# Kernel tuning notes

Measured on AMD Instinct MI355X. Metric: run time of the kernel, lower is better.

## Reference

```python
import jax, jax.numpy as jnp
import numpy as np

B, T, C = 2, 2048, 1024
H, HD = 16, 64
M = 256  # per memory bank
K_CANON = 4


def setup_inputs() -> dict:
    key = jax.random.key(0)
    ks = jax.random.split(key, 10)
    s = 0.02
    return {
        "x": jax.random.normal(ks[0], (B, T, C), jnp.float32),
        "fwd_mem": jax.random.normal(ks[1], (B, M, C), jnp.float32),
        "rev_mem": jax.random.normal(ks[2], (B, M, C), jnp.float32),
        "Wq": jax.random.normal(ks[3], (C, C), jnp.float32) * s,
        "Wk": jax.random.normal(ks[4], (C, C), jnp.float32) * s,
        "Wv": jax.random.normal(ks[5], (C, C), jnp.float32) * s,
        "Wo": jax.random.normal(ks[6], (C, C), jnp.float32) * s,
        "gate_w": jax.random.normal(ks[7], (H, C), jnp.float32) * s,
        "gate_b": jnp.zeros((H,), jnp.float32),
        "canon_w": jax.random.normal(ks[8], (C, 1, K_CANON), jnp.float32) * s,
        "canon_bias": jax.random.normal(ks[9], (C,), jnp.float32) * s,
    }


def _canon_conv(y, canon_w, canon_bias):
    # causal depthwise conv1d with residual; torch weight [C,1,K] -> WIO kernel [K,1,C]
    kern = jnp.transpose(canon_w, (2, 1, 0))
    y_pad = jnp.pad(y, ((0, 0), (K_CANON - 1, 0), (0, 0)))
    conv = jax.lax.conv_general_dilated(
        y_pad, kern, window_strides=(1,), padding='VALID',
        dimension_numbers=('NWC', 'WIO', 'NWC'), feature_group_count=C)
    return y + conv + canon_bias


def reference(x, fwd_mem, rev_mem, Wq, Wk, Wv, Wo, gate_w, gate_b, canon_w, canon_bias):
    Bn, Tn, Cn = x.shape
    scale = 1.0 / np.sqrt(HD)

    q = x @ Wq.T  # [B,T,C]
    k = x @ Wk.T
    v = x @ Wv.T
    # memory integration: project memories with same k/v proj, concat on seq dim
    k = jnp.concatenate([k, fwd_mem @ Wk.T, rev_mem @ Wk.T], axis=1)  # [B,S,C]
    v = jnp.concatenate([v, fwd_mem @ Wv.T, rev_mem @ Wv.T], axis=1)
    S = k.shape[1]
    mem_len = S - Tn

    def heads(t):
        return t.reshape(Bn, -1, H, HD).transpose(0, 2, 1, 3)  # [B,h,S,hd]

    qh, kh, vh = heads(q), heads(k), heads(v)
    scores = jnp.einsum('bhtd,bhsd->bhts', qh, kh) * scale  # [B,h,T,S]
    # causal mask over the first T key columns; memory columns fully visible
    causal = jnp.triu(jnp.ones((Tn, Tn), bool), k=1)
    full_mask = jnp.pad(causal, ((0, 0), (0, mem_len)))  # [T,S]
    scores = jnp.where(full_mask[None, None], -jnp.inf, scores)
    w = jax.nn.softmax(scores, axis=-1)

    # split chunk vs memory, gate memory contribution per head
    w_chunk, w_mem = w[..., :Tn], w[..., Tn:]
    v_chunk, v_mem = vh[:, :, :Tn], vh[:, :, Tn:]
    Y_chunk = jnp.einsum('bhts,bhsd->bhtd', w_chunk, v_chunk)
    Y_mem = jnp.einsum('bhtm,bhmd->bhtd', w_mem, v_mem)
    g = jax.nn.sigmoid(q @ gate_w.T + gate_b)  # [B,T,h]
    g = g.transpose(0, 2, 1)[..., None]  # [B,h,T,1]
    Y = Y_chunk + g * Y_mem

    attn_out = Y.transpose(0, 2, 1, 3).reshape(Bn, Tn, Cn)
    attn_out = _canon_conv(attn_out, canon_w, canon_bias)
    return attn_out @ Wo.T
```

## Files before the change

### kernel.cpp

```cpp
#include <hip/hip_runtime.h>
#include <hip/hip_bf16.h>
#include <cstdint>


typedef __bf16 bf16x8_t __attribute__((ext_vector_type(8)));
typedef __bf16 bf16x4_t __attribute__((ext_vector_type(4)));
typedef float f32x4_t __attribute__((ext_vector_type(4)));

__device__ __forceinline__ f32x4_t mfma16(bf16x8_t a, bf16x8_t b, f32x4_t c) {
    return __builtin_amdgcn_mfma_f32_16x16x32_bf16(a, b, c, 0, 0, 0);
}

__device__ __forceinline__ void gl2lds16(const void* g, void* l) {
    __builtin_amdgcn_global_load_lds(
        (__attribute__((address_space(1))) uint32_t*)(uintptr_t)g,
        (__attribute__((address_space(3))) uint32_t*)l, 16, 0, 0);
}

#define OFF_X   0
#define OFF_FWD 4194304
#define OFF_REV 4718592
#define OFF_WQ  5242880
#define OFF_WK  6291456
#define OFF_WV  7340032
#define OFF_WO  8388608
#define OFF_GW  9437184
#define OFF_GB  9453568
#define OFF_CW  9453584
#define OFF_CB  9457680
#define N_TOT   9458704

__global__ __launch_bounds__(256) void conv_all_kernel(
    const void* p0, const void* p1, const void* p2, const void* p3,
    const void* p4, const void* p5, const void* p6, const void* p7,
    const void* p8, const void* p9, const void* p10,
    __hip_bfloat16* __restrict__ arena)
{
    const int i = (blockIdx.x * 256 + threadIdx.x) * 4;
    if (i >= N_TOT) return;
    const void* src; int off;
    if      (i < OFF_FWD) { src = p0;  off = OFF_X;   }
    else if (i < OFF_REV) { src = p1;  off = OFF_FWD; }
    else if (i < OFF_WQ)  { src = p2;  off = OFF_REV; }
    else if (i < OFF_WK)  { src = p3;  off = OFF_WQ;  }
    else if (i < OFF_WV)  { src = p4;  off = OFF_WK;  }
    else if (i < OFF_WO)  { src = p5;  off = OFF_WV;  }
    else if (i < OFF_GW)  { src = p6;  off = OFF_WO;  }
    else if (i < OFF_GB)  { src = p7;  off = OFF_GW;  }
    else if (i < OFF_CW)  { src = p8;  off = OFF_GB;  }
    else if (i < OFF_CB)  { src = p9;  off = OFF_CW;  }
    else                  { src = p10; off = OFF_CB;  }
    const int j = i - off;
    const float4 f = *(const float4*)((const float*)src + j);
    arena[i + 0] = __float2bfloat16(f.x);
    arena[i + 1] = __float2bfloat16(f.y);
    arena[i + 2] = __float2bfloat16(f.z);
    arena[i + 3] = __float2bfloat16(f.w);
}

__device__ __forceinline__ void gemm_core(
    const __hip_bfloat16* __restrict__ A, const __hip_bfloat16* __restrict__ B,
    void* __restrict__ C, int ldc, int f32o, int arow0, int brow0,
    __hip_bfloat16* As, __hip_bfloat16* Bs)
{
    const int tid  = threadIdx.x;
    const int lane = tid & 63;
    const int wid  = tid >> 6;
    const int q4   = lane >> 4;
    const int c16  = lane & 15;
    const int wm   = (wid >> 1) * 64;
    const int wn   = (wid & 1) * 64;
    const int c0 = tid;
    const int c1 = tid + 256;
    const __hip_bfloat16* gA0 = A + (size_t)(arow0 + (c0 >> 2)) * 1024 + ((c0 & 3) << 3);
    const __hip_bfloat16* gA1 = A + (size_t)(arow0 + (c1 >> 2)) * 1024 + ((c1 & 3) << 3);
    const __hip_bfloat16* gB0 = B + (size_t)(brow0 + (c0 >> 2)) * 1024 + ((c0 & 3) << 3);
    const __hip_bfloat16* gB1 = B + (size_t)(brow0 + (c1 >> 2)) * 1024 + ((c1 & 3) << 3);

    f32x4_t acc[4][4];
#pragma unroll
    for (int i = 0; i < 4; ++i)
#pragma unroll
        for (int j = 0; j < 4; ++j)
#pragma unroll
            for (int r = 0; r < 4; ++r) acc[i][j][r] = 0.0f;

    gl2lds16(gA0, As + c0 * 8);
    gl2lds16(gA1, As + c1 * 8);
    gl2lds16(gB0, Bs + c0 * 8);
    gl2lds16(gB1, Bs + c1 * 8);

    for (int it = 0; it < 32; ++it) {
        __hip_bfloat16* curA = As + (it & 1) * 4096;
        __hip_bfloat16* curB = Bs + (it & 1) * 4096;
        __syncthreads();
        if (it < 31) {
            const int nk = (it + 1) * 32;
            __hip_bfloat16* nA = As + ((it + 1) & 1) * 4096;
            __hip_bfloat16* nB = Bs + ((it + 1) & 1) * 4096;
            gl2lds16(gA0 + nk, nA + c0 * 8);
            gl2lds16(gA1 + nk, nA + c1 * 8);
            gl2lds16(gB0 + nk, nB + c0 * 8);
            gl2lds16(gB1 + nk, nB + c1 * 8);
        }
        bf16x8_t af[4], bfr[4];
#pragma unroll
        for (int i = 0; i < 4; ++i)
            af[i] = *(const bf16x8_t*)&curA[(wm + i * 16 + c16) * 32 + q4 * 8];
#pragma unroll
        for (int j = 0; j < 4; ++j)
            bfr[j] = *(const bf16x8_t*)&curB[(wn + j * 16 + c16) * 32 + q4 * 8];
#pragma unroll
        for (int i = 0; i < 4; ++i)
#pragma unroll
            for (int j = 0; j < 4; ++j)
                acc[i][j] = mfma16(af[i], bfr[j], acc[i][j]);
    }
#pragma unroll
    for (int i = 0; i < 4; ++i) {
        const int mg = arow0 + wm + i * 16 + q4 * 4;
#pragma unroll
        for (int j = 0; j < 4; ++j) {
            const int ng = brow0 + wn + j * 16 + c16;
#pragma unroll
            for (int r = 0; r < 4; ++r) {
                const size_t idx = (size_t)(mg + r) * ldc + ng;
                if (f32o) ((float*)C)[idx] = acc[i][j][r];
                else ((__hip_bfloat16*)C)[idx] = __float2bfloat16(acc[i][j][r]);
            }
        }
    }
}

__global__ __launch_bounds__(256) void qkv_kernel(
    const __hip_bfloat16* __restrict__ x, const __hip_bfloat16* __restrict__ Wqk,
    const __hip_bfloat16* __restrict__ Wv,
    __hip_bfloat16* __restrict__ QK, __hip_bfloat16* __restrict__ Vt)
{
    __shared__ __align__(16) __hip_bfloat16 As[2 * 128 * 32];
    __shared__ __align__(16) __hip_bfloat16 Bs[2 * 128 * 32];
    int id = blockIdx.x;
    if (id < 640)
        gemm_core(x, Wqk, QK, 2048, 0, (id >> 4) * 128, (id & 15) * 128, As, Bs);
    else {
        id -= 640;
        gemm_core(Wv, x, Vt, 5120, 0, (id & 7) * 128, (id >> 3) * 128, As, Bs);
    }
}

__global__ __launch_bounds__(256) void gemm_bt_kernel(
    const __hip_bfloat16* __restrict__ A, const __hip_bfloat16* __restrict__ B,
    void* __restrict__ C, int ldc, int f32o)
{
    __shared__ __align__(16) __hip_bfloat16 As[2 * 128 * 32];
    __shared__ __align__(16) __hip_bfloat16 Bs[2 * 128 * 32];
    gemm_core(A, B, C, ldc, f32o, blockIdx.x * 128, blockIdx.y * 128, As, Bs);
}

__global__ __launch_bounds__(64) void gate_kernel(
    const __hip_bfloat16* __restrict__ QK, const __hip_bfloat16* __restrict__ gw,
    const __hip_bfloat16* __restrict__ gb, float* __restrict__ G)
{
    const int base = blockIdx.x * 16;
    const int lane = threadIdx.x;
    const int q4   = lane >> 4;
    const int c16  = lane & 15;
    f32x4_t acc = {0.0f, 0.0f, 0.0f, 0.0f};
    const __hip_bfloat16* qrow = QK + (size_t)(base + c16) * 2048 + q4 * 8;
    const __hip_bfloat16* wrow = gw + (size_t)c16 * 1024 + q4 * 8;
#pragma unroll
    for (int kk = 0; kk < 32; ++kk) {
        const bf16x8_t a = *(const bf16x8_t*)(qrow + kk * 32);
        const bf16x8_t w = *(const bf16x8_t*)(wrow + kk * 32);
        acc = mfma16(a, w, acc);
    }
    const float bias = __bfloat162float(gb[c16]);
#pragma unroll
    for (int r = 0; r < 4; ++r) {
        const int row = base + q4 * 4 + r;
        G[(size_t)row * 16 + c16] = 1.0f / (1.0f + __expf(-(acc[r] + bias)));
    }
}

#define PSTR 72
__global__ __launch_bounds__(256) void attn_kernel(
    const __hip_bfloat16* __restrict__ QK,
    const __hip_bfloat16* __restrict__ Vt,
    const float* __restrict__ G, __hip_bfloat16* __restrict__ Y)
{
    __shared__ __align__(16) __hip_bfloat16 Ks[64 * 64];
    __shared__ __align__(16) __hip_bfloat16 Vs[64 * 64];
    __shared__ __align__(16) __hip_bfloat16 Plds[4][16 * PSTR];
    const int flat = blockIdx.x;
    const int bh   = flat & 31;
    const int tIdx = 31 - (flat >> 5);
    const int b    = bh >> 4;
    const int h    = bh & 15;
    const int tid  = threadIdx.x;
    const int wid  = tid >> 6;
    const int lane = tid & 63;
    const int q4   = lane >> 4;
    const int c16  = lane & 15;
    const int rowbase = tIdx * 64 + wid * 16;

    const __hip_bfloat16* qrow = QK + (size_t)(b * 2048 + rowbase + c16) * 2048 + h * 64;
    const bf16x8_t qa0 = *(const bf16x8_t*)(qrow + q4 * 8);
    const bf16x8_t qa1 = *(const bf16x8_t*)(qrow + 32 + q4 * 8);

    float rs[4], gate[4];
    f32x4_t acc[4];
#pragma unroll
    for (int fp = 0; fp < 4; ++fp)
#pragma unroll
        for (int r = 0; r < 4; ++r) acc[fp][r] = 0.0f;
#pragma unroll
    for (int r = 0; r < 4; ++r) {
        rs[r] = 0.0f;
        gate[r] = G[(size_t)(b * 2048 + rowbase + q4 * 4 + r) * 16 + h];
    }

    const int nCausal = tIdx + 1;
    const int nTiles  = nCausal + 8;
    auto kvRow = [&](int tile) -> int {
        if (tile < nCausal) return b * 2048 + tile * 64;
        const int mi = (tile - nCausal) * 64;
        return (mi < 256) ? 4096 + b * 256 + mi : 4608 + b * 256 + (mi - 256);
    };

    const int srow0 = tid >> 3,         sch0 = (tid & 7) ^ (srow0 & 7);
    const int srow1 = (tid + 256) >> 3, sch1 = (tid & 7) ^ (srow1 & 7);
    const int sw0 = (q4 ^ (c16 & 7)) * 8;
    const int sw1 = ((q4 + 4) ^ (c16 & 7)) * 8;
    const __hip_bfloat16* Kbase = QK + 1024 + h * 64;

    for (int tile = 0; tile < nTiles; ++tile) {
        const bool isMem  = (tile >= nCausal);
        const bool isDiag = (tile == nCausal - 1);
        const int  vr     = kvRow(tile);
        __syncthreads();
        gl2lds16(Kbase + (size_t)(vr + srow0) * 2048 + sch0 * 8, &Ks[tid * 8]);
        gl2lds16(Kbase + (size_t)(vr + srow1) * 2048 + sch1 * 8, &Ks[(tid + 256) * 8]);
        gl2lds16(Vt + (size_t)(h * 64 + srow0) * 5120 + vr + sch0 * 8, &Vs[tid * 8]);
        gl2lds16(Vt + (size_t)(h * 64 + srow1) * 5120 + vr + sch1 * 8, &Vs[(tid + 256) * 8]);
        __syncthreads();
        bf16x8_t kb0[4], kb1[4], vb0[4], vb1[4];
#pragma unroll
        for (int f = 0; f < 4; ++f) {
            kb0[f] = *(const bf16x8_t*)&Ks[(f * 16 + c16) * 64 + sw0];
            kb1[f] = *(const bf16x8_t*)&Ks[(f * 16 + c16) * 64 + sw1];
            vb0[f] = *(const bf16x8_t*)&Vs[(f * 16 + c16) * 64 + sw0];
            vb1[f] = *(const bf16x8_t*)&Vs[(f * 16 + c16) * 64 + sw1];
        }
        f32x4_t sc[4];
#pragma unroll
        for (int f = 0; f < 4; ++f) {
            f32x4_t z = {0.0f, 0.0f, 0.0f, 0.0f};
            z = mfma16(qa0, kb0[f], z);
            z = mfma16(qa1, kb1[f], z);
            sc[f] = z;
        }
#pragma unroll
        for (int f = 0; f < 4; ++f)
#pragma unroll
            for (int r = 0; r < 4; ++r) {
                float p = __expf(sc[f][r] * 0.125f);
                if (isDiag) {
                    const int sg = tile * 64 + f * 16 + c16;
                    if (sg > rowbase + q4 * 4 + r) p = 0.0f;
                }
                rs[r] += p;
                if (isMem) p *= gate[r];
                Plds[wid][(q4 * 4 + r) * PSTR + f * 16 + c16] = __float2bfloat16(p);
            }
        const bf16x8_t pa0 = *(const bf16x8_t*)&Plds[wid][c16 * PSTR + q4 * 8];
        const bf16x8_t pa1 = *(const bf16x8_t*)&Plds[wid][c16 * PSTR + 32 + q4 * 8];
#pragma unroll
        for (int fp = 0; fp < 4; ++fp) {
            acc[fp] = mfma16(pa0, vb0[fp], acc[fp]);
            acc[fp] = mfma16(pa1, vb1[fp], acc[fp]);
        }
    }
#pragma unroll
    for (int m = 1; m <= 8; m <<= 1)
#pragma unroll
        for (int r = 0; r < 4; ++r) rs[r] += __shfl_xor(rs[r], m, 64);
    float inv[4];
#pragma unroll
    for (int r = 0; r < 4; ++r) inv[r] = 1.0f / rs[r];
#pragma unroll
    for (int fp = 0; fp < 4; ++fp)
#pragma unroll
        for (int r = 0; r < 4; ++r) {
            const int tg = rowbase + q4 * 4 + r;
            Y[(size_t)(b * 2048 + tg) * 1024 + h * 64 + fp * 16 + c16] =
                __float2bfloat16(acc[fp][r] * inv[r]);
        }
}

__global__ __launch_bounds__(256) void canon_kernel(
    const __hip_bfloat16* __restrict__ Yin, const __hip_bfloat16* __restrict__ cw,
    const __hip_bfloat16* __restrict__ cb, __hip_bfloat16* __restrict__ Yout)
{
    const int idx = (blockIdx.x * 256 + threadIdx.x) * 4;
    const int c = idx & 1023;
    const int t = (idx >> 10) & 2047;
    const bf16x4_t y0 = *(const bf16x4_t*)(Yin + idx);
    const bf16x4_t bb = *(const bf16x4_t*)(cb + c);
    float a[4];
#pragma unroll
    for (int i = 0; i < 4; ++i) a[i] = (float)y0[i] + (float)bb[i];
    const bf16x8_t w01 = *(const bf16x8_t*)(cw + c * 4);
    const bf16x8_t w23 = *(const bf16x8_t*)(cw + c * 4 + 8);
#pragma unroll
    for (int j = 0; j < 4; ++j) {
        if (t - 3 + j >= 0) {
            const bf16x4_t yj = *(const bf16x4_t*)(Yin + idx + (j - 3) * 1024);
            a[0] += (float)yj[0] * (float)w01[j];
            a[1] += (float)yj[1] * (float)w01[4 + j];
            a[2] += (float)yj[2] * (float)w23[j];
            a[3] += (float)yj[3] * (float)w23[4 + j];
        }
    }
    bf16x4_t o;
#pragma unroll
    for (int i = 0; i < 4; ++i) o[i] = (__bf16)a[i];
    *(bf16x4_t*)(Yout + idx) = o;
}

extern "C" void kernel_launch(void* const* d_in, const int* in_sizes, int n_in,
                              void* d_out, int out_size, void* d_ws, size_t ws_size,
                              hipStream_t stream)
{
    char* ws = (char*)d_ws;
    const size_t MB = 1ull << 20;
    if (ws_size < 50 * MB) return;

    __hip_bfloat16* arena = (__hip_bfloat16*)ws;
    __hip_bfloat16* QK    = (__hip_bfloat16*)(ws + 19 * MB);
    __hip_bfloat16* Vt    = (__hip_bfloat16*)(ws + 39 * MB);
    float*          G     = (float*)(ws + 49 * MB);
    __hip_bfloat16* Y1    = (__hip_bfloat16*)ws;
    __hip_bfloat16* Y2    = QK;

    const dim3 blk(256);
    conv_all_kernel<<<dim3((N_TOT / 4 + 255) / 256), blk, 0, stream>>>(
        d_in[0], d_in[1], d_in[2], d_in[3], d_in[4], d_in[5], d_in[6],
        d_in[7], d_in[8], d_in[9], d_in[10], arena);

    const __hip_bfloat16* xB  = arena + OFF_X;
    const __hip_bfloat16* WqB = arena + OFF_WQ;
    const __hip_bfloat16* WvB = arena + OFF_WV;
    const __hip_bfloat16* WoB = arena + OFF_WO;

    qkv_kernel<<<dim3(960), blk, 0, stream>>>(xB, WqB, WvB, QK, Vt);
    gate_kernel<<<dim3(256), dim3(64), 0, stream>>>(QK, arena + OFF_GW, arena + OFF_GB, G);
    attn_kernel<<<dim3(1024), blk, 0, stream>>>(QK, Vt, G, Y1);
    canon_kernel<<<dim3(4096), blk, 0, stream>>>(Y1, arena + OFF_CW, arena + OFF_CB, Y2);
    gemm_bt_kernel<<<dim3(32, 8), blk, 0, stream>>>(Y2, WoB, d_out, 1024, 1);
}
```

Measured before the change: 240.1 us.

## Double query rows per attention block and transpose MFMA operands for K/V reuse

Each attention block now covers 128 query rows (32 per wave, two 16-row groups), which halves the grid and doubles reuse of each K/V tile loaded into LDS. The score and PV MFMAs are transposed (K/V as the A operand) so probabilities come out in a layout that allows vectorized bf16x4 LDS writes and output stores. Row sums are reduced across fewer lanes. Waves whose causal range has already ended skip compute on tiles past their diagonal, but they still take part in the loads and barriers, so some waves sit idle on those tiles. The larger tile also raises register pressure and leaves fewer blocks to balance the causal work across.

```diff
diff --git a/kernel.cpp b/kernel.cpp
--- a/kernel.cpp
+++ b/kernel.cpp
@@ -190,10 +190,10 @@
 {
     __shared__ __align__(16) __hip_bfloat16 Ks[64 * 64];
     __shared__ __align__(16) __hip_bfloat16 Vs[64 * 64];
-    __shared__ __align__(16) __hip_bfloat16 Plds[4][16 * PSTR];
+    __shared__ __align__(16) __hip_bfloat16 Pq[4][32 * PSTR];
     const int flat = blockIdx.x;
     const int bh   = flat & 31;
-    const int tIdx = 31 - (flat >> 5);
+    const int tIdx = 15 - (flat >> 5);
     const int b    = bh >> 4;
     const int h    = bh & 15;
     const int tid  = threadIdx.x;
@@ -201,25 +201,29 @@
     const int lane = tid & 63;
     const int q4   = lane >> 4;
     const int c16  = lane & 15;
-    const int rowbase = tIdx * 64 + wid * 16;
-
-    const __hip_bfloat16* qrow = QK + (size_t)(b * 2048 + rowbase + c16) * 2048 + h * 64;
-    const bf16x8_t qa0 = *(const bf16x8_t*)(qrow + q4 * 8);
-    const bf16x8_t qa1 = *(const bf16x8_t*)(qrow + 32 + q4 * 8);
-
-    float rs[4], gate[4];
-    f32x4_t acc[4];
+    const int rowbase = tIdx * 128 + wid * 32;
+    const int dTile   = rowbase >> 6;
+
+    bf16x8_t qa[2][2];
+    int tok[2]; float gate[2], rs[2];
+#pragma unroll
+    for (int qg = 0; qg < 2; ++qg) {
+        tok[qg] = rowbase + qg * 16 + c16;
+        const __hip_bfloat16* qrow = QK + (size_t)(b * 2048 + tok[qg]) * 2048 + h * 64;
+        qa[qg][0] = *(const bf16x8_t*)(qrow + q4 * 8);
+        qa[qg][1] = *(const bf16x8_t*)(qrow + 32 + q4 * 8);
+        gate[qg] = G[(size_t)(b * 2048 + tok[qg]) * 16 + h];
+        rs[qg] = 0.0f;
+    }
+    f32x4_t acc[4][2];
 #pragma unroll
     for (int fp = 0; fp < 4; ++fp)
 #pragma unroll
-        for (int r = 0; r < 4; ++r) acc[fp][r] = 0.0f;
-#pragma unroll
-    for (int r = 0; r < 4; ++r) {
-        rs[r] = 0.0f;
-        gate[r] = G[(size_t)(b * 2048 + rowbase + q4 * 4 + r) * 16 + h];
-    }
-
-    const int nCausal = tIdx + 1;
+        for (int qg = 0; qg < 2; ++qg)
+#pragma unroll
+            for (int r = 0; r < 4; ++r) acc[fp][qg][r] = 0.0f;
+
+    const int nCausal = 2 * tIdx + 2;
     const int nTiles  = nCausal + 8;
     auto kvRow = [&](int tile) -> int {
         if (tile < nCausal) return b * 2048 + tile * 64;
@@ -235,7 +239,8 @@
 
     for (int tile = 0; tile < nTiles; ++tile) {
         const bool isMem  = (tile >= nCausal);
-        const bool isDiag = (tile == nCausal - 1);
+        const bool isDiag = (tile == dTile);
+        const bool active = isMem || (tile <= dTile);
         const int  vr     = kvRow(tile);
         __syncthreads();
         gl2lds16(Kbase + (size_t)(vr + srow0) * 2048 + sch0 * 8, &Ks[tid * 8]);
@@ -243,6 +248,7 @@
         gl2lds16(Vt + (size_t)(h * 64 + srow0) * 5120 + vr + sch0 * 8, &Vs[tid * 8]);
         gl2lds16(Vt + (size_t)(h * 64 + srow1) * 5120 + vr + sch1 * 8, &Vs[(tid + 256) * 8]);
         __syncthreads();
+        if (!active) continue;
         bf16x8_t kb0[4], kb1[4], vb0[4], vb1[4];
 #pragma unroll
         for (int f = 0; f < 4; ++f) {
@@ -251,49 +257,56 @@
             vb0[f] = *(const bf16x8_t*)&Vs[(f * 16 + c16) * 64 + sw0];
             vb1[f] = *(const bf16x8_t*)&Vs[(f * 16 + c16) * 64 + sw1];
         }
-        f32x4_t sc[4];
-#pragma unroll
-        for (int f = 0; f < 4; ++f) {
-            f32x4_t z = {0.0f, 0.0f, 0.0f, 0.0f};
-            z = mfma16(qa0, kb0[f], z);
-            z = mfma16(qa1, kb1[f], z);
-            sc[f] = z;
-        }
 #pragma unroll
         for (int f = 0; f < 4; ++f)
 #pragma unroll
-            for (int r = 0; r < 4; ++r) {
-                float p = __expf(sc[f][r] * 0.125f);
-                if (isDiag) {
-                    const int sg = tile * 64 + f * 16 + c16;
-                    if (sg > rowbase + q4 * 4 + r) p = 0.0f;
+            for (int qg = 0; qg < 2; ++qg) {
+                f32x4_t z = {0.0f, 0.0f, 0.0f, 0.0f};
+                z = mfma16(kb0[f], qa[qg][0], z);
+                z = mfma16(kb1[f], qa[qg][1], z);
+                bf16x4_t pk;
+#pragma unroll
+                for (int r = 0; r < 4; ++r) {
+                    float p = __expf(z[r] * 0.125f);
+                    if (isDiag) {
+                        const int kg = tile * 64 + f * 16 + q4 * 4 + r;
+                        if (kg > tok[qg]) p = 0.0f;
+                    }
+                    rs[qg] += p;
+                    if (isMem) p *= gate[qg];
+                    pk[r] = (__bf16)p;
                 }
-                rs[r] += p;
-                if (isMem) p *= gate[r];
-                Plds[wid][(q4 * 4 + r) * PSTR + f * 16 + c16] = __float2bfloat16(p);
+                *(bf16x4_t*)&Pq[wid][(qg * 16 + c16) * PSTR + f * 16 + q4 * 4] = pk;
             }
-        const bf16x8_t pa0 = *(const bf16x8_t*)&Plds[wid][c16 * PSTR + q4 * 8];
-        const bf16x8_t pa1 = *(const bf16x8_t*)&Plds[wid][c16 * PSTR + 32 + q4 * 8];
-#pragma unroll
-        for (int fp = 0; fp < 4; ++fp) {
-            acc[fp] = mfma16(pa0, vb0[fp], acc[fp]);
-            acc[fp] = mfma16(pa1, vb1[fp], acc[fp]);
-        }
-    }
-#pragma unroll
-    for (int m = 1; m <= 8; m <<= 1)
-#pragma unroll
-        for (int r = 0; r < 4; ++r) rs[r] += __shfl_xor(rs[r], m, 64);
-    float inv[4];
-#pragma unroll
-    for (int r = 0; r < 4; ++r) inv[r] = 1.0f / rs[r];
+        bf16x8_t pb[2][2];
+#pragma unroll
+        for (int qg = 0; qg < 2; ++qg) {
+            pb[qg][0] = *(const bf16x8_t*)&Pq[wid][(qg * 16 + c16) * PSTR + q4 * 8];
+            pb[qg][1] = *(const bf16x8_t*)&Pq[wid][(qg * 16 + c16) * PSTR + 32 + q4 * 8];
+        }
+#pragma unroll
+        for (int fp = 0; fp < 4; ++fp)
+#pragma unroll
+            for (int qg = 0; qg < 2; ++qg) {
+                acc[fp][qg] = mfma16(vb0[fp], pb[qg][0], acc[fp][qg]);
+                acc[fp][qg] = mfma16(vb1[fp], pb[qg][1], acc[fp][qg]);
+            }
+    }
+#pragma unroll
+    for (int qg = 0; qg < 2; ++qg) {
+        rs[qg] += __shfl_xor(rs[qg], 16, 64);
+        rs[qg] += __shfl_xor(rs[qg], 32, 64);
+    }
+    const float inv0 = 1.0f / rs[0], inv1 = 1.0f / rs[1];
 #pragma unroll
     for (int fp = 0; fp < 4; ++fp)
 #pragma unroll
-        for (int r = 0; r < 4; ++r) {
-            const int tg = rowbase + q4 * 4 + r;
-            Y[(size_t)(b * 2048 + tg) * 1024 + h * 64 + fp * 16 + c16] =
-                __float2bfloat16(acc[fp][r] * inv[r]);
+        for (int qg = 0; qg < 2; ++qg) {
+            const float inv = qg ? inv1 : inv0;
+            bf16x4_t o;
+#pragma unroll
+            for (int r = 0; r < 4; ++r) o[r] = (__bf16)(acc[fp][qg][r] * inv);
+            *(bf16x4_t*)&Y[(size_t)(b * 2048 + tok[qg]) * 1024 + h * 64 + fp * 16 + q4 * 4] = o;
         }
 }
 
@@ -354,7 +367,7 @@
 
     qkv_kernel<<<dim3(960), blk, 0, stream>>>(xB, WqB, WvB, QK, Vt);
     gate_kernel<<<dim3(256), dim3(64), 0, stream>>>(QK, arena + OFF_GW, arena + OFF_GB, G);
-    attn_kernel<<<dim3(1024), blk, 0, stream>>>(QK, Vt, G, Y1);
+    attn_kernel<<<dim3(512), blk, 0, stream>>>(QK, Vt, G, Y1);
     canon_kernel<<<dim3(4096), blk, 0, stream>>>(Y1, arena + OFF_CW, arena + OFF_CB, Y2);
     gemm_bt_kernel<<<dim3(32, 8), blk, 0, stream>>>(Y2, WoB, d_out, 1024, 1);
 }
```

Result: slower. 254.2 us (+5.9%).

## Give each attention wave 32 query rows and halve block to 128 threads

Applied to the files above, without the earlier changes.

The attention kernel now runs 2 waves per block instead of 4, and each wave handles two 16-row query groups. The K/V fragments it reads from LDS are reused across both groups, which halves LDS fragment reads per query row. Each block still covers 64 query rows, so tile loads are now spread over fewer threads (4 loads each). In exchange, each wave holds more registers (two accumulator sets and a larger P buffer), which may lower occupancy, and there are fewer waves per block to hide latency.

```diff
diff --git a/kernel.cpp b/kernel.cpp
--- a/kernel.cpp
+++ b/kernel.cpp
@@ -183,14 +183,14 @@
 }
 
 #define PSTR 72
-__global__ __launch_bounds__(256) void attn_kernel(
+__global__ __launch_bounds__(128) void attn_kernel(
     const __hip_bfloat16* __restrict__ QK,
     const __hip_bfloat16* __restrict__ Vt,
     const float* __restrict__ G, __hip_bfloat16* __restrict__ Y)
 {
     __shared__ __align__(16) __hip_bfloat16 Ks[64 * 64];
     __shared__ __align__(16) __hip_bfloat16 Vs[64 * 64];
-    __shared__ __align__(16) __hip_bfloat16 Plds[4][16 * PSTR];
+    __shared__ __align__(16) __hip_bfloat16 Pq[2][32 * PSTR];
     const int flat = blockIdx.x;
     const int bh   = flat & 31;
     const int tIdx = 31 - (flat >> 5);
@@ -201,23 +201,30 @@
     const int lane = tid & 63;
     const int q4   = lane >> 4;
     const int c16  = lane & 15;
-    const int rowbase = tIdx * 64 + wid * 16;
-
-    const __hip_bfloat16* qrow = QK + (size_t)(b * 2048 + rowbase + c16) * 2048 + h * 64;
-    const bf16x8_t qa0 = *(const bf16x8_t*)(qrow + q4 * 8);
-    const bf16x8_t qa1 = *(const bf16x8_t*)(qrow + 32 + q4 * 8);
-
-    float rs[4], gate[4];
-    f32x4_t acc[4];
+    const int rowbase = tIdx * 64 + wid * 32;
+
+    bf16x8_t qa[2][2];
+    float rs[2][4], gate[2][4];
+    f32x4_t acc[4][2];
+#pragma unroll
+    for (int mg = 0; mg < 2; ++mg) {
+        const __hip_bfloat16* qrow =
+            QK + (size_t)(b * 2048 + rowbase + mg * 16 + c16) * 2048 + h * 64;
+        qa[mg][0] = *(const bf16x8_t*)(qrow + q4 * 8);
+        qa[mg][1] = *(const bf16x8_t*)(qrow + 32 + q4 * 8);
+#pragma unroll
+        for (int r = 0; r < 4; ++r) {
+            rs[mg][r] = 0.0f;
+            gate[mg][r] =
+                G[(size_t)(b * 2048 + rowbase + mg * 16 + q4 * 4 + r) * 16 + h];
+        }
+    }
 #pragma unroll
     for (int fp = 0; fp < 4; ++fp)
 #pragma unroll
-        for (int r = 0; r < 4; ++r) acc[fp][r] = 0.0f;
-#pragma unroll
-    for (int r = 0; r < 4; ++r) {
-        rs[r] = 0.0f;
-        gate[r] = G[(size_t)(b * 2048 + rowbase + q4 * 4 + r) * 16 + h];
-    }
+        for (int mg = 0; mg < 2; ++mg)
+#pragma unroll
+            for (int r = 0; r < 4; ++r) acc[fp][mg][r] = 0.0f;
 
     const int nCausal = tIdx + 1;
     const int nTiles  = nCausal + 8;
@@ -227,8 +234,13 @@
         return (mi < 256) ? 4096 + b * 256 + mi : 4608 + b * 256 + (mi - 256);
     };
 
-    const int srow0 = tid >> 3,         sch0 = (tid & 7) ^ (srow0 & 7);
-    const int srow1 = (tid + 256) >> 3, sch1 = (tid & 7) ^ (srow1 & 7);
+    int srow[4], sch[4];
+#pragma unroll
+    for (int i = 0; i < 4; ++i) {
+        const int s = i * 128 + tid;
+        srow[i] = s >> 3;
+        sch[i]  = (s & 7) ^ (srow[i] & 7);
+    }
     const int sw0 = (q4 ^ (c16 & 7)) * 8;
     const int sw1 = ((q4 + 4) ^ (c16 & 7)) * 8;
     const __hip_bfloat16* Kbase = QK + 1024 + h * 64;
@@ -238,10 +250,13 @@
         const bool isDiag = (tile == nCausal - 1);
         const int  vr     = kvRow(tile);
         __syncthreads();
-        gl2lds16(Kbase + (size_t)(vr + srow0) * 2048 + sch0 * 8, &Ks[tid * 8]);
-        gl2lds16(Kbase + (size_t)(vr + srow1) * 2048 + sch1 * 8, &Ks[(tid + 256) * 8]);
-        gl2lds16(Vt + (size_t)(h * 64 + srow0) * 5120 + vr + sch0 * 8, &Vs[tid * 8]);
-        gl2lds16(Vt + (size_t)(h * 64 + srow1) * 5120 + vr + sch1 * 8, &Vs[(tid + 256) * 8]);
+#pragma unroll
+        for (int i = 0; i < 4; ++i) {
+            gl2lds16(Kbase + (size_t)(vr + srow[i]) * 2048 + sch[i] * 8,
+                     &Ks[(i * 128 + tid) * 8]);
+            gl2lds16(Vt + (size_t)(h * 64 + srow[i]) * 5120 + vr + sch[i] * 8,
+                     &Vs[(i * 128 + tid) * 8]);
+        }
         __syncthreads();
         bf16x8_t kb0[4], kb1[4], vb0[4], vb1[4];
 #pragma unroll
@@ -251,50 +266,62 @@
             vb0[f] = *(const bf16x8_t*)&Vs[(f * 16 + c16) * 64 + sw0];
             vb1[f] = *(const bf16x8_t*)&Vs[(f * 16 + c16) * 64 + sw1];
         }
-        f32x4_t sc[4];
-#pragma unroll
-        for (int f = 0; f < 4; ++f) {
-            f32x4_t z = {0.0f, 0.0f, 0.0f, 0.0f};
-            z = mfma16(qa0, kb0[f], z);
-            z = mfma16(qa1, kb1[f], z);
-            sc[f] = z;
-        }
 #pragma unroll
         for (int f = 0; f < 4; ++f)
 #pragma unroll
+            for (int mg = 0; mg < 2; ++mg) {
+                f32x4_t z = {0.0f, 0.0f, 0.0f, 0.0f};
+                z = mfma16(qa[mg][0], kb0[f], z);
+                z = mfma16(qa[mg][1], kb1[f], z);
+#pragma unroll
+                for (int r = 0; r < 4; ++r) {
+                    float p = __expf(z[r] * 0.125f);
+                    if (isDiag) {
+                        const int kg = tile * 64 + f * 16 + c16;
+                        if (kg > rowbase + mg * 16 + q4 * 4 + r) p = 0.0f;
+                    }
+                    rs[mg][r] += p;
+                    if (isMem) p *= gate[mg][r];
+                    Pq[wid][(mg * 16 + q4 * 4 + r) * PSTR + f * 16 + c16] =
+                        __float2bfloat16(p);
+                }
+            }
+        bf16x8_t pa[2][2];
+#pragma unroll
+        for (int mg = 0; mg < 2; ++mg) {
+            pa[mg][0] = *(const bf16x8_t*)&Pq[wid][(mg * 16 + c16) * PSTR + q4 * 8];
+            pa[mg][1] = *(const bf16x8_t*)&Pq[wid][(mg * 16 + c16) * PSTR + 32 + q4 * 8];
+        }
+#pragma unroll
+        for (int fp = 0; fp < 4; ++fp)
+#pragma unroll
+            for (int mg = 0; mg < 2; ++mg) {
+                acc[fp][mg] = mfma16(pa[mg][0], vb0[fp], acc[fp][mg]);
+                acc[fp][mg] = mfma16(pa[mg][1], vb1[fp], acc[fp][mg]);
+            }
+    }
+#pragma unroll
+    for (int m = 1; m <= 8; m <<= 1)
+#pragma unroll
+        for (int mg = 0; mg < 2; ++mg)
+#pragma unroll
+            for (int r = 0; r < 4; ++r)
+                rs[mg][r] += __shfl_xor(rs[mg][r], m, 64);
+    float inv[2][4];
+#pragma unroll
+    for (int mg = 0; mg < 2; ++mg)
+#pragma unroll
+        for (int r = 0; r < 4; ++r) inv[mg][r] = 1.0f / rs[mg][r];
+#pragma unroll
+    for (int fp = 0; fp < 4; ++fp)
+#pragma unroll
+        for (int mg = 0; mg < 2; ++mg)
+#pragma unroll
             for (int r = 0; r < 4; ++r) {
-                float p = __expf(sc[f][r] * 0.125f);
-                if (isDiag) {
-                    const int sg = tile * 64 + f * 16 + c16;
-                    if (sg > rowbase + q4 * 4 + r) p = 0.0f;
-                }
-                rs[r] += p;
-                if (isMem) p *= gate[r];
-                Plds[wid][(q4 * 4 + r) * PSTR + f * 16 + c16] = __float2bfloat16(p);
+                const int tg = rowbase + mg * 16 + q4 * 4 + r;
+                Y[(size_t)(b * 2048 + tg) * 1024 + h * 64 + fp * 16 + c16] =
+                    __float2bfloat16(acc[fp][mg][r] * inv[mg][r]);
             }
-        const bf16x8_t pa0 = *(const bf16x8_t*)&Plds[wid][c16 * PSTR + q4 * 8];
-        const bf16x8_t pa1 = *(const bf16x8_t*)&Plds[wid][c16 * PSTR + 32 + q4 * 8];
-#pragma unroll
-        for (int fp = 0; fp < 4; ++fp) {
-            acc[fp] = mfma16(pa0, vb0[fp], acc[fp]);
-            acc[fp] = mfma16(pa1, vb1[fp], acc[fp]);
-        }
-    }
-#pragma unroll
-    for (int m = 1; m <= 8; m <<= 1)
-#pragma unroll
-        for (int r = 0; r < 4; ++r) rs[r] += __shfl_xor(rs[r], m, 64);
-    float inv[4];
-#pragma unroll
-    for (int r = 0; r < 4; ++r) inv[r] = 1.0f / rs[r];
-#pragma unroll
-    for (int fp = 0; fp < 4; ++fp)
-#pragma unroll
-        for (int r = 0; r < 4; ++r) {
-            const int tg = rowbase + q4 * 4 + r;
-            Y[(size_t)(b * 2048 + tg) * 1024 + h * 64 + fp * 16 + c16] =
-                __float2bfloat16(acc[fp][r] * inv[r]);
-        }
 }
 
 __global__ __launch_bounds__(256) void canon_kernel(
@@ -354,7 +381,7 @@
 
     qkv_kernel<<<dim3(960), blk, 0, stream>>>(xB, WqB, WvB, QK, Vt);
     gate_kernel<<<dim3(256), dim3(64), 0, stream>>>(QK, arena + OFF_GW, arena + OFF_GB, G);
-    attn_kernel<<<dim3(1024), blk, 0, stream>>>(QK, Vt, G, Y1);
+    attn_kernel<<<dim3(1024), dim3(128), 0, stream>>>(QK, Vt, G, Y1);
     canon_kernel<<<dim3(4096), blk, 0, stream>>>(Y1, arena + OFF_CW, arena + OFF_CB, Y2);
     gemm_bt_kernel<<<dim3(32, 8), blk, 0, stream>>>(Y2, WoB, d_out, 1024, 1);
 }
```

New measurement: 256.1 us. 6.7% more time.
